# Performance work log

Hardware: AMD Instinct MI355X
Metric: run time of the kernel (lower is better)

## Reference

```python
import jax, jax.numpy as jnp
import numpy as np

HIDDEN = 4096
N_HEADS = 32
N_KV = 32
HEAD_DIM = HIDDEN // N_HEADS  # 128
T = 2048
THETA = 10000.0
EPS = 1e-5


def setup_inputs() -> dict:
    key = jax.random.key(0)
    ks = jax.random.split(key, 7)
    s = 0.02
    return {
        "positions": jnp.arange(T, dtype=jnp.int64),
        "hidden_states": jax.random.normal(ks[0], (T, HIDDEN), jnp.float32),
        "w_qkv": jax.random.normal(ks[1], ((N_HEADS + 2 * N_KV) * HEAD_DIM, HIDDEN), jnp.float32) * s,
        "w_o": jax.random.normal(ks[2], (HIDDEN, N_HEADS * HEAD_DIM), jnp.float32) * s,
        "q_norm_w": jnp.ones((N_HEADS, HEAD_DIM), jnp.float32) + jax.random.normal(ks[3], (N_HEADS, HEAD_DIM), jnp.float32) * s,
        "q_norm_b": jax.random.normal(ks[4], (N_HEADS, HEAD_DIM), jnp.float32) * s,
        "k_norm_w": jnp.ones((N_KV, HEAD_DIM), jnp.float32) + jax.random.normal(ks[5], (N_KV, HEAD_DIM), jnp.float32) * s,
        "k_norm_b": jax.random.normal(ks[6], (N_KV, HEAD_DIM), jnp.float32) * s,
    }


def _layer_norm_affine(x, w, b):
    # x: [T, H, d]; normalize over last dim, no affine inside, then per-head affine
    mu = jnp.mean(x, axis=-1, keepdims=True)
    var = jnp.var(x, axis=-1, keepdims=True)
    xn = (x - mu) * jax.lax.rsqrt(var + EPS)
    return xn * w + b


def _rope_neox(x, positions):
    # x: [T, H, d], NEOX style: rotate halves over full head_dim
    half = HEAD_DIM // 2
    inv_freq = 1.0 / (THETA ** (jnp.arange(0, half, dtype=jnp.float32) * 2.0 / HEAD_DIM))
    ang = positions.astype(jnp.float32)[:, None] * inv_freq  # [T, half]
    cos = jnp.cos(ang)[:, None, :]
    sin = jnp.sin(ang)[:, None, :]
    x1, x2 = x[..., :half], x[..., half:]
    return jnp.concatenate([x1 * cos - x2 * sin, x2 * cos + x1 * sin], axis=-1)


def reference(positions, hidden_states, w_qkv, w_o, q_norm_w, q_norm_b, k_norm_w, k_norm_b):
    qkv = hidden_states @ w_qkv.T  # [T, (H+2Hkv)*d]
    q_size = N_HEADS * HEAD_DIM
    kv_size = N_KV * HEAD_DIM
    q = qkv[:, :q_size].reshape(T, N_HEADS, HEAD_DIM)
    k = qkv[:, q_size:q_size + kv_size].reshape(T, N_KV, HEAD_DIM)
    v = qkv[:, q_size + kv_size:].reshape(T, N_KV, HEAD_DIM)

    q = _layer_norm_affine(q, q_norm_w, q_norm_b)
    k = _layer_norm_affine(k, k_norm_w, k_norm_b)
    q = _rope_neox(q, positions)
    k = _rope_neox(k, positions)

    scale = HEAD_DIM ** -0.5
    scores = jnp.einsum('thd,shd->hts', q, k) * scale  # [H, T, T]
    causal = jnp.tril(jnp.ones((T, T), dtype=bool))
    scores = jnp.where(causal[None], scores, jnp.finfo(scores.dtype).min)
    p = jax.nn.softmax(scores, axis=-1)
    attn = jnp.einsum('hts,shd->thd', p, v).reshape(T, N_HEADS * HEAD_DIM)
    return attn @ w_o.T
```

## Files before the change

### kernel.cpp

```cpp
#include <hip/hip_runtime.h>
#include <cstdint>

#define T_SEQ 2048
#define HID   4096
#define NH    32
#define HD    128
#define QKVW  12288

typedef float  f32x4  __attribute__((ext_vector_type(4)));
typedef __bf16 bf16x8 __attribute__((ext_vector_type(8)));

#define QSCALE (0.08838834764831845f * 1.4426950408889634f)

__device__ __forceinline__ unsigned short f2bf(float f) {
  unsigned int u = __builtin_bit_cast(unsigned int, f);
  u += 0x7fffu + ((u >> 16) & 1u);
  return (unsigned short)(u >> 16);
}

__device__ __forceinline__ void gload_lds16(const void* gptr, void* lptr) {
  __builtin_amdgcn_global_load_lds(
      (const __attribute__((address_space(1))) unsigned int*)(unsigned long long)(uintptr_t)gptr,
      (__attribute__((address_space(3))) unsigned int*)(unsigned int)(uintptr_t)lptr,
      16, 0, 0);
}

__global__ __launch_bounds__(256) void cast_bf16(const float* __restrict__ in,
                                                 unsigned short* __restrict__ out,
                                                 int n4) {
  int i = blockIdx.x * 256 + threadIdx.x;
  int stride = gridDim.x * 256;
  for (; i < n4; i += stride) {
    float4 v = ((const float4*)in)[i];
    ushort4 o;
    o.x = f2bf(v.x); o.y = f2bf(v.y); o.z = f2bf(v.z); o.w = f2bf(v.w);
    ((ushort4*)out)[i] = o;
  }
}

__global__ __launch_bounds__(512, 2) void gemm_bt(const unsigned short* __restrict__ Ag,
                                                  const unsigned short* __restrict__ Bg,
                                                  float* __restrict__ C,
                                                  int M, int N, int K, int MT) {
  __shared__ unsigned short As_[2][128 * 64];
  __shared__ unsigned short Bs_[2][256 * 64];
  const int tid  = threadIdx.x;
  const int lane = tid & 63;
  const int w    = tid >> 6;
  const int wm   = w >> 2;
  const int wn   = w & 3;
  const int l15  = lane & 15;
  const int lg   = lane >> 4;

  const int nwg = gridDim.x;
  const int cpx = nwg >> 3;
  const int swz = (blockIdx.x & 7) * cpx + (blockIdx.x >> 3);
  const int bm  = (swz % MT) * 128;
  const int bn  = (swz / MT) * 256;
  const int nk  = K >> 6;

#define STAGE_A(buf, kt_) do {                                                   \
    const unsigned short* _s = Ag + (size_t)bm * K + (size_t)(kt_) * 64;         \
    _Pragma("unroll")                                                            \
    for (int _u = 0; _u < 2; ++_u) {                                             \
      const int _cid = _u * 512 + tid;                                           \
      const int _r = _cid >> 3, _ch = _cid & 7;                                  \
      gload_lds16(_s + (size_t)_r * K + ((_ch ^ (_r & 7)) * 8),                  \
                  &As_[buf][(_u * 512 + w * 64) * 8]);                           \
    } } while (0)

#define STAGE_B(buf, kt_) do {                                                   \
    const unsigned short* _s = Bg + (size_t)bn * K + (size_t)(kt_) * 64;         \
    _Pragma("unroll")                                                            \
    for (int _u = 0; _u < 4; ++_u) {                                             \
      const int _cid = _u * 512 + tid;                                           \
      const int _r = _cid >> 3, _ch = _cid & 7;                                  \
      gload_lds16(_s + (size_t)_r * K + ((_ch ^ (_r & 7)) * 8),                  \
                  &Bs_[buf][(_u * 512 + w * 64) * 8]);                           \
    } } while (0)

  f32x4 acc[4][4] = {};

  STAGE_A(0, 0);
  STAGE_B(0, 0);
  if (nk > 1) {
    STAGE_B(1, 1);
    asm volatile("s_waitcnt vmcnt(4)" ::: "memory");
  } else {
    asm volatile("s_waitcnt vmcnt(0)" ::: "memory");
  }
  __builtin_amdgcn_s_barrier();

  for (int t = 0; t < nk; ++t) {
    const int cur = t & 1;
    bf16x8 bfr[4][2];
#pragma unroll
    for (int n = 0; n < 4; ++n)
#pragma unroll
      for (int kk = 0; kk < 2; ++kk) {
        const int r = wn * 64 + n * 16 + l15;
        bfr[n][kk] = *(const bf16x8*)&Bs_[cur][r * 64 + (((kk * 4 + lg) ^ (r & 7)) * 8)];
      }
    bf16x8 a0[2][2];
#pragma unroll
    for (int mi = 0; mi < 2; ++mi)
#pragma unroll
      for (int kk = 0; kk < 2; ++kk) {
        const int r = wm * 64 + mi * 16 + l15;
        a0[mi][kk] = *(const bf16x8*)&As_[cur][r * 64 + (((kk * 4 + lg) ^ (r & 7)) * 8)];
      }
    if (t + 1 < nk) STAGE_A(cur ^ 1, t + 1);
    __builtin_amdgcn_s_barrier();
    __builtin_amdgcn_s_setprio(1);
#pragma unroll
    for (int mi = 0; mi < 2; ++mi)
#pragma unroll
      for (int n = 0; n < 4; ++n)
#pragma unroll
        for (int kk = 0; kk < 2; ++kk)
          acc[mi][n] = __builtin_amdgcn_mfma_f32_16x16x32_bf16(a0[mi][kk], bfr[n][kk], acc[mi][n], 0, 0, 0);
    __builtin_amdgcn_s_setprio(0);
    __builtin_amdgcn_s_barrier();

    bf16x8 a1[2][2];
#pragma unroll
    for (int mi = 0; mi < 2; ++mi)
#pragma unroll
      for (int kk = 0; kk < 2; ++kk) {
        const int r = wm * 64 + (2 + mi) * 16 + l15;
        a1[mi][kk] = *(const bf16x8*)&As_[cur][r * 64 + (((kk * 4 + lg) ^ (r & 7)) * 8)];
      }
    if (t + 2 < nk) STAGE_B(cur, t + 2);
    __builtin_amdgcn_s_barrier();
    __builtin_amdgcn_s_setprio(1);
#pragma unroll
    for (int mi = 0; mi < 2; ++mi)
#pragma unroll
      for (int n = 0; n < 4; ++n)
#pragma unroll
        for (int kk = 0; kk < 2; ++kk)
          acc[2 + mi][n] = __builtin_amdgcn_mfma_f32_16x16x32_bf16(a1[mi][kk], bfr[n][kk], acc[2 + mi][n], 0, 0, 0);
    __builtin_amdgcn_s_setprio(0);
    if (t + 1 < nk) {
      if (t + 2 < nk) asm volatile("s_waitcnt vmcnt(4)" ::: "memory");
      else            asm volatile("s_waitcnt vmcnt(0)" ::: "memory");
      __builtin_amdgcn_sched_barrier(0);
    }
    __builtin_amdgcn_s_barrier();
  }
#undef STAGE_A
#undef STAGE_B

#pragma unroll
  for (int m = 0; m < 4; ++m)
#pragma unroll
    for (int i = 0; i < 4; ++i) {
      const int row = bm + wm * 64 + m * 16 + lg * 4 + i;
#pragma unroll
      for (int n = 0; n < 4; ++n)
        C[(size_t)row * N + bn + wn * 64 + n * 16 + l15] = acc[m][n][i];
    }
}

__global__ __launch_bounds__(512, 2) void gemm_bt8(const unsigned short* __restrict__ Ag,
                                                   const unsigned short* __restrict__ Bg,
                                                   float* __restrict__ C,
                                                   int M, int N, int K, int MT) {
  __shared__ unsigned short As_[2][256 * 64];
  __shared__ unsigned short Bs_[2][256 * 64];
  const int tid  = threadIdx.x;
  const int lane = tid & 63;
  const int w    = tid >> 6;
  const int wm   = w >> 2;
  const int wn   = w & 3;
  const int l15  = lane & 15;
  const int lg   = lane >> 4;
  const int sw   = l15 & 7;

  const int cpx = gridDim.x >> 3;
  const int swz = (blockIdx.x & 7) * cpx + (blockIdx.x >> 3);
  const int bm  = (swz % MT) * 256;
  const int bn  = (swz / MT) * 256;
  const int nk  = K >> 6;

  const unsigned short* Abase = Ag + (size_t)bm * K;
  const unsigned short* Bbase = Bg + (size_t)bn * K;

#define SG(ldsbase, gbase, kt_, u_) do {                                        \
    const int _cid = (u_) * 512 + tid;                                          \
    const int _r = _cid >> 3, _ch = _cid & 7;                                   \
    gload_lds16((gbase) + (size_t)_r * K + (size_t)(kt_) * 64 +                 \
                    ((_ch ^ (_r & 7)) * 8),                                     \
                (void*)((char*)(ldsbase) + _cid * 16));                         \
  } while (0)

#define RD(base, r, kk)                                                          \
  (*(const bf16x8*)((const char*)(base) + (r) * 128 + ((((kk) * 4 + lg) ^ sw) * 16)))

#define MFMA16(mbase, bfr) do {                                                  \
    _Pragma("unroll")                                                            \
    for (int _m = 0; _m < 4; ++_m)                                               \
      _Pragma("unroll")                                                          \
      for (int _n = 0; _n < 4; ++_n)                                             \
        acc[(mbase) + _m][_n] = __builtin_amdgcn_mfma_f32_16x16x32_bf16(         \
            aP[_m], bfr[_n], acc[(mbase) + _m][_n], 0, 0, 0);                    \
  } while (0)

  f32x4 acc[8][4] = {};

#pragma unroll
  for (int u = 0; u < 4; ++u) SG(As_[0], Abase, 0, u);
#pragma unroll
  for (int u = 0; u < 4; ++u) SG(Bs_[0], Bbase, 0, u);
  if (nk > 1) {
    SG(As_[1], Abase, 1, 0); SG(As_[1], Abase, 1, 2);
    SG(Bs_[1], Bbase, 1, 0); SG(Bs_[1], Bbase, 1, 1);
    SG(Bs_[1], Bbase, 1, 2); SG(Bs_[1], Bbase, 1, 3);
    asm volatile("s_waitcnt vmcnt(6)" ::: "memory");
  } else {
    asm volatile("s_waitcnt vmcnt(0)" ::: "memory");
  }
  __builtin_amdgcn_sched_barrier(0);
  __builtin_amdgcn_s_barrier();

  for (int t = 0; t < nk; ++t) {
    const int cur = t & 1;
    const unsigned short* As = As_[cur];
    const unsigned short* Bs = Bs_[cur];
    bf16x8 bfr0[4], bfr1[4], aP[4];

#pragma unroll
    for (int m = 0; m < 4; ++m) aP[m] = RD(As, wm * 128 + m * 16 + l15, 0);
#pragma unroll
    for (int n = 0; n < 4; ++n) bfr0[n] = RD(Bs, wn * 64 + n * 16 + l15, 0);
    if (t + 1 < nk) { SG(As_[cur ^ 1], Abase, t + 1, 1); SG(As_[cur ^ 1], Abase, t + 1, 3); }
    __builtin_amdgcn_s_barrier();
    asm volatile("s_waitcnt lgkmcnt(0)" ::: "memory");
    __builtin_amdgcn_sched_barrier(0);
    __builtin_amdgcn_s_setprio(1);
    MFMA16(0, bfr0);
    __builtin_amdgcn_s_setprio(0);
    __builtin_amdgcn_s_barrier();

#pragma unroll
    for (int m = 0; m < 4; ++m) aP[m] = RD(As, wm * 128 + m * 16 + l15, 1);
#pragma unroll
    for (int n = 0; n < 4; ++n) bfr1[n] = RD(Bs, wn * 64 + n * 16 + l15, 1);
    __builtin_amdgcn_s_barrier();
    asm volatile("s_waitcnt lgkmcnt(0)" ::: "memory");
    __builtin_amdgcn_sched_barrier(0);
    __builtin_amdgcn_s_setprio(1);
    MFMA16(0, bfr1);
    __builtin_amdgcn_s_setprio(0);
    asm volatile("s_waitcnt vmcnt(8)" ::: "memory");
    __builtin_amdgcn_sched_barrier(0);
    __builtin_amdgcn_s_barrier();

#pragma unroll
    for (int m = 0; m < 4; ++m) aP[m] = RD(As, wm * 128 + (4 + m) * 16 + l15, 0);
    if (t + 2 < nk) {
      SG(As_[cur], Abase, t + 2, 0); SG(As_[cur], Abase, t + 2, 2);
      SG(Bs_[cur], Bbase, t + 2, 0); SG(Bs_[cur], Bbase, t + 2, 1);
    }
    __builtin_amdgcn_s_barrier();
    asm volatile("s_waitcnt lgkmcnt(0)" ::: "memory");
    __builtin_amdgcn_sched_barrier(0);
    __builtin_amdgcn_s_setprio(1);
    MFMA16(4, bfr0);
    __builtin_amdgcn_s_setprio(0);
    __builtin_amdgcn_s_barrier();

#pragma unroll
    for (int m = 0; m < 4; ++m) aP[m] = RD(As, wm * 128 + (4 + m) * 16 + l15, 1);
    if (t + 2 < nk) { SG(Bs_[cur], Bbase, t + 2, 2); SG(Bs_[cur], Bbase, t + 2, 3); }
    __builtin_amdgcn_s_barrier();
    asm volatile("s_waitcnt lgkmcnt(0)" ::: "memory");
    __builtin_amdgcn_sched_barrier(0);
    __builtin_amdgcn_s_setprio(1);
    MFMA16(4, bfr1);
    __builtin_amdgcn_s_setprio(0);
    if (t + 1 < nk) {
      if (t + 2 < nk) asm volatile("s_waitcnt vmcnt(8)" ::: "memory");
      else            asm volatile("s_waitcnt vmcnt(0)" ::: "memory");
      __builtin_amdgcn_sched_barrier(0);
    }
    __builtin_amdgcn_s_barrier();
  }
#undef SG
#undef RD
#undef MFMA16

#pragma unroll
  for (int m = 0; m < 8; ++m)
#pragma unroll
    for (int i = 0; i < 4; ++i) {
      const int row = bm + wm * 128 + m * 16 + lg * 4 + i;
#pragma unroll
      for (int n = 0; n < 4; ++n)
        C[(size_t)row * N + bn + wn * 64 + n * 16 + l15] = acc[m][n][i];
    }
}

__global__ __launch_bounds__(256) void norm_rope(const float* __restrict__ qkv,
                                                 const float* __restrict__ qw,
                                                 const float* __restrict__ qb,
                                                 const float* __restrict__ kw,
                                                 const float* __restrict__ kb,
                                                 unsigned short* __restrict__ q,
                                                 unsigned short* __restrict__ k,
                                                 unsigned short* __restrict__ v) {
  const int t    = blockIdx.x;
  const int tid  = threadIdx.x;
  const int lane = tid & 63;
  const int w    = tid >> 6;
  const float invf = exp2f(-(float)lane * (13.287712379549449f / 64.0f));
  const float ang  = (float)t * invf;
  const float c = cosf(ang), s = sinf(ang);
  const float* row = qkv + (size_t)t * QKVW;

#pragma unroll 1
  for (int sel = 0; sel < 2; ++sel) {
    const float* src = row + sel * HID;
    const float* wgt = sel ? kw : qw;
    const float* bia = sel ? kb : qb;
    unsigned short* dst = sel ? k : q;
    const float oscale = sel ? 1.0f : QSCALE;
    for (int h = w; h < NH; h += 4) {
      const float* x = src + h * HD;
      float x1 = x[lane], x2 = x[lane + 64];
      float sum = x1 + x2, ss = x1 * x1 + x2 * x2;
#pragma unroll
      for (int m = 1; m < 64; m <<= 1) {
        sum += __shfl_xor(sum, m, 64);
        ss  += __shfl_xor(ss, m, 64);
      }
      const float mu  = sum * (1.0f / 128.0f);
      const float var = ss * (1.0f / 128.0f) - mu * mu;
      const float r   = rsqrtf(var + 1e-5f);
      const float n1  = (x1 - mu) * r * wgt[h * HD + lane]      + bia[h * HD + lane];
      const float n2  = (x2 - mu) * r * wgt[h * HD + lane + 64] + bia[h * HD + lane + 64];
      const float o1  = (n1 * c - n2 * s) * oscale;
      const float o2  = (n2 * c + n1 * s) * oscale;
      dst[(size_t)t * HID + h * HD + lane]      = f2bf(o1);
      dst[(size_t)t * HID + h * HD + lane + 64] = f2bf(o2);
    }
  }
  const float* vx = row + 2 * HID;
  unsigned short* vdst = v + (size_t)t * HID;
  for (int j = tid; j < HID / 4; j += 256) {
    float4 val = ((const float4*)vx)[j];
    ushort4 o;
    o.x = f2bf(val.x); o.y = f2bf(val.y); o.z = f2bf(val.z); o.w = f2bf(val.w);
    ((ushort4*)vdst)[j] = o;
  }
}

__global__ __launch_bounds__(256) void transpose_v(const unsigned short* __restrict__ v,
                                                   unsigned short* __restrict__ vt) {
  __shared__ unsigned short tile[64][65];
  const int h  = blockIdx.z;
  const int tt = blockIdx.x * 64;
  const int dd = blockIdx.y * 64;
  const int tid = threadIdx.x;
#pragma unroll
  for (int p = 0; p < 4; ++p) {
    int idx = p * 256 + tid;
    int r = idx >> 4, c4 = idx & 15;
    ushort4 val = *(const ushort4*)&v[(size_t)(tt + r) * HID + h * HD + dd + c4 * 4];
    tile[r][c4 * 4 + 0] = val.x;
    tile[r][c4 * 4 + 1] = val.y;
    tile[r][c4 * 4 + 2] = val.z;
    tile[r][c4 * 4 + 3] = val.w;
  }
  __syncthreads();
#pragma unroll
  for (int p = 0; p < 4; ++p) {
    int idx = p * 256 + tid;
    int r = idx >> 4, c4 = idx & 15;
    ushort4 o;
    o.x = tile[c4 * 4 + 0][r];
    o.y = tile[c4 * 4 + 1][r];
    o.z = tile[c4 * 4 + 2][r];
    o.w = tile[c4 * 4 + 3][r];
    *(ushort4*)&vt[((size_t)h * HD + dd + r) * T_SEQ + tt + c4 * 4] = o;
  }
}

__global__ __launch_bounds__(256) void attn_fwd(const unsigned short* __restrict__ Q,
                                                const unsigned short* __restrict__ K,
                                                const unsigned short* __restrict__ VT,
                                                unsigned short* __restrict__ O) {
  __shared__ unsigned short Ks[2][64 * 128];
  __shared__ unsigned short Vs[2][128 * 64];
  __shared__ unsigned short Ps[4][16 * 64];
  const int h    = blockIdx.y;
  const int pair = blockIdx.x;
  const int tid  = threadIdx.x;
  const int lane = tid & 63;
  const int w    = tid >> 6;
  const int l15  = lane & 15;
  const int lg   = lane >> 4;
  const int sw   = l15 & 7;

#pragma unroll 1
  for (int half = 0; half < 2; ++half) {
    const int qt   = half ? (31 - pair) : pair;
    const int qrow = qt * 64 + w * 16;

    bf16x8 qf[4];
#pragma unroll
    for (int kk = 0; kk < 4; ++kk)
      qf[kk] = *(const bf16x8*)&Q[(size_t)(qrow + l15) * HID + h * HD + kk * 32 + lg * 8];

    f32x4 o[8] = {};
    float mrow[4], lrow[4];
#pragma unroll
    for (int i = 0; i < 4; ++i) { mrow[i] = -1e30f; lrow[i] = 0.0f; }

    const int nkt = qt + 1;

    {
#pragma unroll
      for (int p = 0; p < 4; ++p) {
        const int c  = p * 256 + tid;
        const int kr = c >> 4, kc = c & 15;
        gload_lds16(&K[(size_t)kr * HID + h * HD + ((kc ^ (kr & 7)) * 8)],
                    &Ks[0][(p * 256 + w * 64) * 8]);
        const int vr = c >> 3, vc = c & 7;
        gload_lds16(&VT[((size_t)h * HD + vr) * T_SEQ + ((vc ^ (vr & 7)) * 8)],
                    &Vs[0][(p * 256 + w * 64) * 8]);
      }
    }
    __syncthreads();

#pragma unroll 1
    for (int kt = 0; kt < nkt; ++kt) {
      const int cur = kt & 1;
      if (kt + 1 < nkt) {
        const int k0 = (kt + 1) * 64;
#pragma unroll
        for (int p = 0; p < 4; ++p) {
          const int c  = p * 256 + tid;
          const int kr = c >> 4, kc = c & 15;
          gload_lds16(&K[(size_t)(k0 + kr) * HID + h * HD + ((kc ^ (kr & 7)) * 8)],
                      &Ks[cur ^ 1][(p * 256 + w * 64) * 8]);
          const int vr = c >> 3, vc = c & 7;
          gload_lds16(&VT[((size_t)h * HD + vr) * T_SEQ + k0 + ((vc ^ (vr & 7)) * 8)],
                      &Vs[cur ^ 1][(p * 256 + w * 64) * 8]);
        }
      }
      const unsigned short* ksb = Ks[cur];
      const unsigned short* vsb = Vs[cur];

      f32x4 sfr[4] = {};
#pragma unroll
      for (int n = 0; n < 4; ++n)
#pragma unroll
        for (int kk = 0; kk < 4; ++kk) {
          bf16x8 kf = *(const bf16x8*)&ksb[(n * 16 + l15) * 128 + ((kk * 4 + lg) ^ sw) * 8];
          sfr[n] = __builtin_amdgcn_mfma_f32_16x16x32_bf16(qf[kk], kf, sfr[n], 0, 0, 0);
        }

      if (kt == qt) {
#pragma unroll
        for (int n = 0; n < 4; ++n)
#pragma unroll
          for (int i = 0; i < 4; ++i)
            if (n * 16 + l15 > w * 16 + lg * 4 + i) sfr[n][i] = -1e30f;
      }

      float escale[4];
#pragma unroll
      for (int i = 0; i < 4; ++i) {
        float mx = fmaxf(fmaxf(sfr[0][i], sfr[1][i]), fmaxf(sfr[2][i], sfr[3][i]));
        mx = fmaxf(mx, __shfl_xor(mx, 1, 64));
        mx = fmaxf(mx, __shfl_xor(mx, 2, 64));
        mx = fmaxf(mx, __shfl_xor(mx, 4, 64));
        mx = fmaxf(mx, __shfl_xor(mx, 8, 64));
        const float mnew = fmaxf(mrow[i], mx);
        escale[i] = exp2f(mrow[i] - mnew);
        mrow[i] = mnew;
        const int prow = lg * 4 + i;
        float rs = 0.0f;
#pragma unroll
        for (int n = 0; n < 4; ++n) {
          const float p = exp2f(sfr[n][i] - mnew);
          rs += p;
          Ps[w][prow * 64 + (((2 * n + (l15 >> 3)) ^ (prow & 7)) * 8) + sw] = f2bf(p);
        }
        rs += __shfl_xor(rs, 1, 64);
        rs += __shfl_xor(rs, 2, 64);
        rs += __shfl_xor(rs, 4, 64);
        rs += __shfl_xor(rs, 8, 64);
        lrow[i] = lrow[i] * escale[i] + rs;
      }
#pragma unroll
      for (int f = 0; f < 8; ++f)
#pragma unroll
        for (int i = 0; i < 4; ++i) o[f][i] *= escale[i];

      asm volatile("s_waitcnt lgkmcnt(0)" ::: "memory");
      __builtin_amdgcn_sched_barrier(0);

      bf16x8 pf[2];
#pragma unroll
      for (int kk = 0; kk < 2; ++kk)
        pf[kk] = *(const bf16x8*)&Ps[w][l15 * 64 + ((kk * 4 + lg) ^ sw) * 8];
#pragma unroll
      for (int f = 0; f < 8; ++f)
#pragma unroll
        for (int kk = 0; kk < 2; ++kk) {
          bf16x8 vf = *(const bf16x8*)&vsb[(f * 16 + l15) * 64 + ((kk * 4 + lg) ^ sw) * 8];
          o[f] = __builtin_amdgcn_mfma_f32_16x16x32_bf16(pf[kk], vf, o[f], 0, 0, 0);
        }

      __syncthreads();
    }

#pragma unroll
    for (int i = 0; i < 4; ++i) {
      const float inv = 1.0f / lrow[i];
      const int trow = qrow + lg * 4 + i;
#pragma unroll
      for (int f = 0; f < 8; ++f)
        O[(size_t)trow * HID + h * HD + f * 16 + l15] = f2bf(o[f][i] * inv);
    }
  }
}

extern "C" void kernel_launch(void* const* d_in, const int* in_sizes, int n_in,
                              void* d_out, int out_size, void* d_ws, size_t ws_size,
                              hipStream_t stream) {
  const float* hidden = (const float*)d_in[1];
  const float* w_qkv  = (const float*)d_in[2];
  const float* w_o    = (const float*)d_in[3];
  const float* qw     = (const float*)d_in[4];
  const float* qb     = (const float*)d_in[5];
  const float* kw     = (const float*)d_in[6];
  const float* kb     = (const float*)d_in[7];

  char* ws = (char*)d_ws;
  unsigned short* wqkv_bf = (unsigned short*)(ws + 0);
  unsigned short* attn_bf = (unsigned short*)(ws + 0);
  unsigned short* wo_bf   = (unsigned short*)(ws + 16777216);
  unsigned short* hid_bf  = (unsigned short*)(ws + 100663296);
  unsigned short* vt_bf   = (unsigned short*)(ws + 100663296);
  float* qkv_f32          = (float*)(ws + 117440512);
  unsigned short* q_bf    = (unsigned short*)(ws + 218103808);
  unsigned short* k_bf    = (unsigned short*)(ws + 234881024);
  unsigned short* v_bf    = (unsigned short*)(ws + 251658240);

  cast_bf16<<<2048, 256, 0, stream>>>(hidden, hid_bf, (T_SEQ * HID) / 4);
  cast_bf16<<<2048, 256, 0, stream>>>(w_qkv, wqkv_bf, (QKVW * HID) / 4);
  gemm_bt8<<<384, 512, 0, stream>>>(hid_bf, wqkv_bf, qkv_f32, T_SEQ, QKVW, HID, 8);
  cast_bf16<<<2048, 256, 0, stream>>>(w_o, wo_bf, (HID * HID) / 4);
  norm_rope<<<T_SEQ, 256, 0, stream>>>(qkv_f32, qw, qb, kw, kb, q_bf, k_bf, v_bf);
  transpose_v<<<dim3(T_SEQ / 64, HD / 64, NH), 256, 0, stream>>>(v_bf, vt_bf);
  attn_fwd<<<dim3(16, NH), 256, 0, stream>>>(q_bf, k_bf, vt_bf, attn_bf);
  gemm_bt<<<256, 512, 0, stream>>>(attn_bf, wo_bf, (float*)d_out, T_SEQ, HID, HID, 16);
}
```

Baseline: 515.4 us.

## Restructure GEMM main loop with register fragments and fewer barriers

The bf16 GEMM main loop now loads all A and B fragments for a k-tile into separate registers (a0–a3, b0, b1). It uses partial lgkmcnt waits so MFMAs can start while later LDS reads are still in flight. Prefetch of the tile two steps ahead is issued as one batch instead of being split across phases, and workgroup barriers drop from about six per iteration to two. This cuts synchronisation stalls and exposes more overlap between LDS reads and MFMA work. In exchange it needs more VGPRs under the 512-thread, 2-block launch bound, and the earlier buffer overwrite may race with other waves' last A-fragment reads.

```diff
diff --git a/kernel.cpp b/kernel.cpp
--- a/kernel.cpp
+++ b/kernel.cpp
@@ -24,6 +24,8 @@
       (__attribute__((address_space(3))) unsigned int*)(unsigned int)(uintptr_t)lptr,
       16, 0, 0);
 }
+
+#define SB __builtin_amdgcn_sched_barrier(0)
 
 __global__ __launch_bounds__(256) void cast_bf16(const float* __restrict__ in,
                                                  unsigned short* __restrict__ out,
@@ -197,13 +199,13 @@
 #define RD(base, r, kk)                                                          \
   (*(const bf16x8*)((const char*)(base) + (r) * 128 + ((((kk) * 4 + lg) ^ sw) * 16)))
 
-#define MFMA16(mbase, bfr) do {                                                  \
+#define MFMA16(mbase, afr, bfr) do {                                             \
     _Pragma("unroll")                                                            \
     for (int _m = 0; _m < 4; ++_m)                                               \
       _Pragma("unroll")                                                          \
       for (int _n = 0; _n < 4; ++_n)                                             \
         acc[(mbase) + _m][_n] = __builtin_amdgcn_mfma_f32_16x16x32_bf16(         \
-            aP[_m], bfr[_n], acc[(mbase) + _m][_n], 0, 0, 0);                    \
+            afr[_m], bfr[_n], acc[(mbase) + _m][_n], 0, 0, 0);                   \
   } while (0)
 
   f32x4 acc[8][4] = {};
@@ -213,78 +215,74 @@
 #pragma unroll
   for (int u = 0; u < 4; ++u) SG(Bs_[0], Bbase, 0, u);
   if (nk > 1) {
-    SG(As_[1], Abase, 1, 0); SG(As_[1], Abase, 1, 2);
-    SG(Bs_[1], Bbase, 1, 0); SG(Bs_[1], Bbase, 1, 1);
-    SG(Bs_[1], Bbase, 1, 2); SG(Bs_[1], Bbase, 1, 3);
-    asm volatile("s_waitcnt vmcnt(6)" ::: "memory");
+#pragma unroll
+    for (int u = 0; u < 4; ++u) SG(As_[1], Abase, 1, u);
+#pragma unroll
+    for (int u = 0; u < 4; ++u) SG(Bs_[1], Bbase, 1, u);
+    asm volatile("s_waitcnt vmcnt(8)" ::: "memory");
   } else {
     asm volatile("s_waitcnt vmcnt(0)" ::: "memory");
   }
-  __builtin_amdgcn_sched_barrier(0);
+  SB;
   __builtin_amdgcn_s_barrier();
 
   for (int t = 0; t < nk; ++t) {
     const int cur = t & 1;
     const unsigned short* As = As_[cur];
     const unsigned short* Bs = Bs_[cur];
-    bf16x8 bfr0[4], bfr1[4], aP[4];
-
-#pragma unroll
-    for (int m = 0; m < 4; ++m) aP[m] = RD(As, wm * 128 + m * 16 + l15, 0);
-#pragma unroll
-    for (int n = 0; n < 4; ++n) bfr0[n] = RD(Bs, wn * 64 + n * 16 + l15, 0);
-    if (t + 1 < nk) { SG(As_[cur ^ 1], Abase, t + 1, 1); SG(As_[cur ^ 1], Abase, t + 1, 3); }
-    __builtin_amdgcn_s_barrier();
-    asm volatile("s_waitcnt lgkmcnt(0)" ::: "memory");
-    __builtin_amdgcn_sched_barrier(0);
+    bf16x8 a0[4], a1[4], a2[4], a3[4], b0[4], b1[4];
+
+#pragma unroll
+    for (int m = 0; m < 4; ++m) a0[m] = RD(As, wm * 128 + m * 16 + l15, 0);
+#pragma unroll
+    for (int n = 0; n < 4; ++n) b0[n] = RD(Bs, wn * 64 + n * 16 + l15, 0);
+    SB;
+#pragma unroll
+    for (int m = 0; m < 4; ++m) a1[m] = RD(As, wm * 128 + m * 16 + l15, 1);
+#pragma unroll
+    for (int n = 0; n < 4; ++n) b1[n] = RD(Bs, wn * 64 + n * 16 + l15, 1);
+    SB;
+    asm volatile("s_waitcnt lgkmcnt(8)" ::: "memory");
+    SB;
     __builtin_amdgcn_s_setprio(1);
-    MFMA16(0, bfr0);
+    MFMA16(0, a0, b0);
+    __builtin_amdgcn_s_setprio(0);
+#pragma unroll
+    for (int m = 0; m < 4; ++m) a2[m] = RD(As, wm * 128 + (4 + m) * 16 + l15, 0);
+    SB;
+    asm volatile("s_waitcnt lgkmcnt(4)" ::: "memory");
+    SB;
+    __builtin_amdgcn_s_setprio(1);
+    MFMA16(0, a1, b1);
     __builtin_amdgcn_s_setprio(0);
     __builtin_amdgcn_s_barrier();
-
-#pragma unroll
-    for (int m = 0; m < 4; ++m) aP[m] = RD(As, wm * 128 + m * 16 + l15, 1);
-#pragma unroll
-    for (int n = 0; n < 4; ++n) bfr1[n] = RD(Bs, wn * 64 + n * 16 + l15, 1);
-    __builtin_amdgcn_s_barrier();
+#pragma unroll
+    for (int m = 0; m < 4; ++m) a3[m] = RD(As, wm * 128 + (4 + m) * 16 + l15, 1);
+    SB;
+    if (t + 2 < nk) {
+#pragma unroll
+      for (int u = 0; u < 4; ++u) SG(As_[cur], Abase, t + 2, u);
+#pragma unroll
+      for (int u = 0; u < 4; ++u) SG(Bs_[cur], Bbase, t + 2, u);
+    }
+    SB;
+    asm volatile("s_waitcnt lgkmcnt(4)" ::: "memory");
+    SB;
+    __builtin_amdgcn_s_setprio(1);
+    MFMA16(4, a2, b0);
+    __builtin_amdgcn_s_setprio(0);
+    SB;
     asm volatile("s_waitcnt lgkmcnt(0)" ::: "memory");
-    __builtin_amdgcn_sched_barrier(0);
+    SB;
     __builtin_amdgcn_s_setprio(1);
-    MFMA16(0, bfr1);
-    __builtin_amdgcn_s_setprio(0);
-    asm volatile("s_waitcnt vmcnt(8)" ::: "memory");
-    __builtin_amdgcn_sched_barrier(0);
-    __builtin_amdgcn_s_barrier();
-
-#pragma unroll
-    for (int m = 0; m < 4; ++m) aP[m] = RD(As, wm * 128 + (4 + m) * 16 + l15, 0);
-    if (t + 2 < nk) {
-      SG(As_[cur], Abase, t + 2, 0); SG(As_[cur], Abase, t + 2, 2);
-      SG(Bs_[cur], Bbase, t + 2, 0); SG(Bs_[cur], Bbase, t + 2, 1);
-    }
-    __builtin_amdgcn_s_barrier();
-    asm volatile("s_waitcnt lgkmcnt(0)" ::: "memory");
-    __builtin_amdgcn_sched_barrier(0);
-    __builtin_amdgcn_s_setprio(1);
-    MFMA16(4, bfr0);
-    __builtin_amdgcn_s_setprio(0);
-    __builtin_amdgcn_s_barrier();
-
-#pragma unroll
-    for (int m = 0; m < 4; ++m) aP[m] = RD(As, wm * 128 + (4 + m) * 16 + l15, 1);
-    if (t + 2 < nk) { SG(Bs_[cur], Bbase, t + 2, 2); SG(Bs_[cur], Bbase, t + 2, 3); }
-    __builtin_amdgcn_s_barrier();
-    asm volatile("s_waitcnt lgkmcnt(0)" ::: "memory");
-    __builtin_amdgcn_sched_barrier(0);
-    __builtin_amdgcn_s_setprio(1);
-    MFMA16(4, bfr1);
+    MFMA16(4, a3, b1);
     __builtin_amdgcn_s_setprio(0);
     if (t + 1 < nk) {
       if (t + 2 < nk) asm volatile("s_waitcnt vmcnt(8)" ::: "memory");
       else            asm volatile("s_waitcnt vmcnt(0)" ::: "memory");
-      __builtin_amdgcn_sched_barrier(0);
-    }
-    __builtin_amdgcn_s_barrier();
+      SB;
+      __builtin_amdgcn_s_barrier();
+    }
   }
 #undef SG
 #undef RD
```

Result: faster. 503.2 us (-2.4%).
